# Performance work log

Hardware: AMD Instinct MI355X
Metric: run time of the kernel (lower is better)

Reference implementation:

```python
import jax, jax.numpy as jnp
import numpy as np

H, D_MODEL, D_K, D_V = 16, 1024, 64, 64
IS_DECODE = True


def setup_inputs() -> dict:
    key = jax.random.key(0)
    ks = jax.random.split(key, 6)
    N, L = 4, 2048
    x = jax.random.normal(ks[0], (N, L, D_MODEL), dtype=jnp.float32)
    masked_info = jnp.ones((N, L), dtype=jnp.float32)  # 1 = valid, 0 = pad
    s = 1.0 / np.sqrt(D_MODEL)
    WQ = jax.random.normal(ks[1], (H, D_MODEL, D_K), dtype=jnp.float32) * s
    WK = jax.random.normal(ks[2], (H, D_MODEL, D_K), dtype=jnp.float32) * s
    WV = jax.random.normal(ks[3], (H, D_MODEL, D_V), dtype=jnp.float32) * s
    WO = jax.random.normal(ks[4], (H * D_V, D_MODEL), dtype=jnp.float32) * s
    return {"x": x, "masked_info": masked_info, "WQ": WQ, "WK": WK, "WV": WV, "WO": WO}


def reference(x, masked_info, WQ, WK, WV, WO):
    N, L, _ = x.shape
    scaler = jnp.sqrt(jnp.array(D_K, dtype=x.dtype))
    # per-head projections, batched over heads: [H, N, L, d]
    q = jnp.einsum('nld,hdk->hnlk', x, WQ)
    k = jnp.einsum('nld,hdk->hnlk', x, WK)
    v = jnp.einsum('nld,hdv->hnlv', x, WV)
    scores = jnp.einsum('hnlk,hnmk->hnlm', q, k) / scaler  # [H, N, L, L]
    # outer-product padding mask: True where masked out
    pad_mask = (masked_info[:, :, None] * masked_info[:, None, :]) == 0  # [N, L, L]
    if IS_DECODE:
        causal = jnp.triu(jnp.ones((L, L), dtype=bool), k=1)
        pad_mask = pad_mask | causal[None, :, :]
    scores = jnp.where(pad_mask[None], -jnp.inf, scores)
    attn = jax.nn.softmax(scores, axis=-1)
    attn = jnp.nan_to_num(attn, nan=0.0)  # rows fully masked -> 0
    out_h = jnp.einsum('hnlm,hnmv->hnlv', attn, v)  # [H, N, L, d_v]
    # concat heads along last dim in head order: [N, L, H*d_v]
    concat = jnp.transpose(out_h, (1, 2, 0, 3)).reshape(N, L, H * D_V)
    return concat @ WO
```

## Files before the change

kernel.cpp:

```cpp
#include <hip/hip_runtime.h>
#include <hip/hip_bf16.h>


typedef unsigned short ushort_t;
typedef __bf16 bf16x8 __attribute__((ext_vector_type(8)));
typedef float  f32x4  __attribute__((ext_vector_type(4)));
typedef unsigned short us4 __attribute__((ext_vector_type(4)));
typedef short s16x4 __attribute__((ext_vector_type(4)));

__device__ __forceinline__ ushort_t f2bf(float f) {
    union { float f; unsigned u; } a; a.f = f;
    unsigned r = a.u + 0x7fffu + ((a.u >> 16) & 1u);
    return (ushort_t)(r >> 16);
}

__device__ __forceinline__ void gload16(const ushort_t* g, ushort_t* l) {
    __builtin_amdgcn_global_load_lds(
        (const __attribute__((address_space(1))) void*)g,
        (__attribute__((address_space(3))) void*)l, 16, 0, 0);
}

__global__ __launch_bounds__(256) void cvt_f32_bf16(const float* __restrict__ in,
                                                    ushort_t* __restrict__ out, int n4) {
    int i = blockIdx.x * 256 + threadIdx.x;
    if (i >= n4) return;
    float4 v = reinterpret_cast<const float4*>(in)[i];
    us4 o;
    o[0] = f2bf(v.x); o[1] = f2bf(v.y); o[2] = f2bf(v.z); o[3] = f2bf(v.w);
    reinterpret_cast<us4*>(out)[i] = o;
}

__global__ __launch_bounds__(256) void cvt_transpose(const float* __restrict__ in,
                                                     ushort_t* __restrict__ out,
                                                     int R, int C, int total) {
    int i = blockIdx.x * 256 + threadIdx.x;
    if (i >= total) return;
    int rc = R * C;
    int b = i / rc; int rem = i - b * rc;
    int c = rem / R; int r = rem - c * R;
    out[i] = f2bf(in[(size_t)(b * R + r) * C + c]);
}

template<int MODE>
__global__ __launch_bounds__(256, 2)
void gemm_bt(const ushort_t* __restrict__ Ag, const ushort_t* __restrict__ BT,
             void* __restrict__ Cout, float scale) {
    const int bm = blockIdx.x, by = blockIdx.y;
    const int tid = threadIdx.x;
    const int w = tid >> 6, lane = tid & 63;
    const int g = lane >> 4, c = lane & 15;
    const int m0 = bm * 128;
    const ushort_t* Bbase = BT + (size_t)by * 65536;

    __shared__ __align__(16) ushort_t As[128 * 64];
    __shared__ __align__(16) ushort_t Bs[64 * 64];

    f32x4 acc[2][4];
    #pragma unroll
    for (int i = 0; i < 2; ++i)
        #pragma unroll
        for (int j = 0; j < 4; ++j) acc[i][j] = (f32x4){0.f, 0.f, 0.f, 0.f};

    const int rsub = (w << 3) + (lane >> 3);
    const int s8   = lane & 7;

    for (int t = 0; t < 16; ++t) {
        const int k0 = t * 64;
        #pragma unroll
        for (int is = 0; is < 4; ++is) {
            const int row = is * 32 + rsub;
            gload16(Ag + (size_t)(m0 + row) * 1024 + k0 + ((s8 ^ (row & 7)) << 3),
                    &As[is * 2048 + w * 512]);
        }
        #pragma unroll
        for (int is = 0; is < 2; ++is) {
            const int row = is * 32 + rsub;
            gload16(Bbase + (size_t)row * 1024 + k0 + ((s8 ^ (row & 7)) << 3),
                    &Bs[is * 2048 + w * 512]);
        }
        __syncthreads();
        #pragma unroll
        for (int kk = 0; kk < 2; ++kk) {
            bf16x8 af[2], bfr[4];
            #pragma unroll
            for (int mf = 0; mf < 2; ++mf) {
                const int row = w * 32 + mf * 16 + c;
                const int slot = (kk * 4 + g) ^ (row & 7);
                af[mf] = *reinterpret_cast<const bf16x8*>(&As[row * 64 + slot * 8]);
            }
            #pragma unroll
            for (int nf = 0; nf < 4; ++nf) {
                const int row = nf * 16 + c;
                const int slot = (kk * 4 + g) ^ (row & 7);
                bfr[nf] = *reinterpret_cast<const bf16x8*>(&Bs[row * 64 + slot * 8]);
            }
            __builtin_amdgcn_s_setprio(1);
            #pragma unroll
            for (int mf = 0; mf < 2; ++mf)
                #pragma unroll
                for (int nf = 0; nf < 4; ++nf)
                    acc[mf][nf] = __builtin_amdgcn_mfma_f32_16x16x32_bf16(
                        af[mf], bfr[nf], acc[mf][nf], 0, 0, 0);
            __builtin_amdgcn_s_setprio(0);
        }
        __syncthreads();
    }

    #pragma unroll
    for (int mf = 0; mf < 2; ++mf) {
        const int mbase = m0 + w * 32 + mf * 16 + g * 4;
        #pragma unroll
        for (int nf = 0; nf < 4; ++nf) {
            const int col = nf * 16 + c;
            if (MODE == 3) {
                ushort_t* o = (ushort_t*)Cout + (size_t)by * 524288;
                if (by < 32) {
                    const float scl = (by < 16) ? scale : 1.0f;
                    #pragma unroll
                    for (int r = 0; r < 4; ++r)
                        o[(size_t)(mbase + r) * 64 + col] = f2bf(acc[mf][nf][r] * scl);
                } else {
                    us4 pk;
                    #pragma unroll
                    for (int r = 0; r < 4; ++r) pk[r] = f2bf(acc[mf][nf][r]);
                    const int nIdx = mbase >> 11, l = mbase & 2047;
                    *reinterpret_cast<us4*>(
                        &o[(size_t)nIdx * 131072 + (size_t)col * 2048 + l]) = pk;
                }
            } else {
                float* o = (float*)Cout;
                #pragma unroll
                for (int r = 0; r < 4; ++r)
                    o[(size_t)(mbase + r) * 1024 + by * 64 + col] = acc[mf][nf][r];
            }
        }
    }
}

__global__ __launch_bounds__(256, 4)
void attn_kernel(const ushort_t* __restrict__ qb, const ushort_t* __restrict__ kb,
                 const ushort_t* __restrict__ vtb, const float* __restrict__ mi,
                 ushort_t* __restrict__ cat) {
    const int bx = blockIdx.x;
    const int n = blockIdx.y, h = blockIdx.z;
    const int tid = threadIdx.x;
    const int w = tid >> 6, lane = tid & 63;
    const int g = lane >> 4, c = lane & 15;
    const int qblkA = bx, qblkB = 31 - bx;
    const int q0A = qblkA * 64 + w * 16;
    const int q0B = qblkB * 64 + w * 16;

    const ushort_t* qhn = qb  + (size_t)h * 524288 + (size_t)n * 131072;
    const ushort_t* khn = kb  + (size_t)h * 524288 + (size_t)n * 131072;
    const ushort_t* vhn = vtb + (size_t)h * 524288 + (size_t)n * 131072;
    const float*    mrow = mi + (size_t)n * 2048;

    __shared__ __align__(16) ushort_t Ks[2][64 * 64];
    __shared__ __align__(16) ushort_t Vs[2][64 * 64];

    const int rsub = (w << 3) + (lane >> 3);
    const int s8   = lane & 7;

    auto stage = [&](int jb, int b) {
        const int kbase = jb * 64;
        #pragma unroll
        for (int is = 0; is < 2; ++is) {
            const int row = is * 32 + rsub;
            const int sg  = (s8 ^ (row & 7)) << 3;
            gload16(khn + (size_t)(kbase + row) * 64 + sg, &Ks[b][is * 2048 + w * 512]);
            gload16(vhn + (size_t)row * 2048 + kbase + sg, &Vs[b][is * 2048 + w * 512]);
        }
    };

    bf16x8 qfA[2], qfB[2];
    {
        const ushort_t* qa = qhn + (size_t)(q0A + c) * 64 + g * 8;
        const ushort_t* qb2 = qhn + (size_t)(q0B + c) * 64 + g * 8;
        qfA[0] = *reinterpret_cast<const bf16x8*>(qa);
        qfA[1] = *reinterpret_cast<const bf16x8*>(qa + 32);
        qfB[0] = *reinterpret_cast<const bf16x8*>(qb2);
        qfB[1] = *reinterpret_cast<const bf16x8*>(qb2 + 32);
    }
    const float mqA = mrow[q0A + c];
    const float mqB = mrow[q0B + c];

    float mrunA = -1e30f, lrunA = 0.f, mrunB = -1e30f, lrunB = 0.f;
    f32x4 accA[4], accB[4];
    #pragma unroll
    for (int i = 0; i < 4; ++i) {
        accA[i] = (f32x4){0.f, 0.f, 0.f, 0.f};
        accB[i] = (f32x4){0.f, 0.f, 0.f, 0.f};
    }

    stage(0, 0);
    __syncthreads();
    int buf = 0;

    for (int j = 0; j <= qblkB; ++j) {
        if (j < qblkB) stage(j + 1, buf ^ 1);
        const int kbase = j * 64;
        f32x4 bias[4];
        #pragma unroll
        for (int nf = 0; nf < 4; ++nf) {
            float4 mk = *reinterpret_cast<const float4*>(&mrow[kbase + nf * 16 + g * 4]);
            bias[nf][0] = (mk.x == 0.f) ? -1e30f : 0.f;
            bias[nf][1] = (mk.y == 0.f) ? -1e30f : 0.f;
            bias[nf][2] = (mk.z == 0.f) ? -1e30f : 0.f;
            bias[nf][3] = (mk.w == 0.f) ? -1e30f : 0.f;
        }

        auto do_pass = [&](const bf16x8* qf, f32x4* acc, float& mrun, float& lrun,
                           int q0, bool diag) {
            f32x4 s[4];
            #pragma unroll
            for (int nf = 0; nf < 4; ++nf) s[nf] = (f32x4){0.f, 0.f, 0.f, 0.f};
            __builtin_amdgcn_s_setprio(1);
            #pragma unroll
            for (int kk = 0; kk < 2; ++kk)
                #pragma unroll
                for (int nf = 0; nf < 4; ++nf) {
                    const int row  = nf * 16 + c;
                    const int byte = row * 128 + (((kk * 4 + g) ^ (c & 7)) << 4);
                    bf16x8 kf = *reinterpret_cast<const bf16x8*>(
                        reinterpret_cast<const char*>(&Ks[buf][0]) + byte);
                    s[nf] = __builtin_amdgcn_mfma_f32_16x16x32_bf16(
                        kf, qf[kk], s[nf], 0, 0, 0);
                }
            __builtin_amdgcn_s_setprio(0);
            #pragma unroll
            for (int nf = 0; nf < 4; ++nf) s[nf] += bias[nf];
            if (diag) {
                const int qrow = q0 + c;
                #pragma unroll
                for (int nf = 0; nf < 4; ++nf)
                    #pragma unroll
                    for (int r = 0; r < 4; ++r)
                        if (kbase + nf * 16 + g * 4 + r > qrow) s[nf][r] = -1e30f;
            }
            float m01[4], m23[4];
            #pragma unroll
            for (int r = 0; r < 4; ++r) {
                m01[r] = fmaxf(s[0][r], s[1][r]);
                m23[r] = fmaxf(s[2][r], s[3][r]);
            }
            float mt = fmaxf(fmaxf(fmaxf(m01[0], m01[1]), fmaxf(m01[2], m01[3])),
                             fmaxf(fmaxf(m23[0], m23[1]), fmaxf(m23[2], m23[3])));
            mt = fmaxf(mt, __shfl_xor(mt, 16));
            mt = fmaxf(mt, __shfl_xor(mt, 32));
            if (!__all(mt - mrun <= 8.0f)) {
                const float mnew = fmaxf(mrun, mt);
                const float sc = __builtin_amdgcn_exp2f(mrun - mnew);
                #pragma unroll
                for (int nfd = 0; nfd < 4; ++nfd)
                    #pragma unroll
                    for (int r = 0; r < 4; ++r) acc[nfd][r] *= sc;
                lrun *= sc;
                mrun = mnew;
            }
            float rs = 0.f;
            union { unsigned u[2]; s16x4 v; } pb[4];
            #pragma unroll
            for (int nf = 0; nf < 4; ++nf) {
                const float p0 = __builtin_amdgcn_exp2f(s[nf][0] - mrun);
                const float p1 = __builtin_amdgcn_exp2f(s[nf][1] - mrun);
                const float p2 = __builtin_amdgcn_exp2f(s[nf][2] - mrun);
                const float p3 = __builtin_amdgcn_exp2f(s[nf][3] - mrun);
                rs += (p0 + p1) + (p2 + p3);
                asm("v_cvt_pk_bf16_f32 %0, %1, %2" : "=v"(pb[nf].u[0]) : "v"(p0), "v"(p1));
                asm("v_cvt_pk_bf16_f32 %0, %1, %2" : "=v"(pb[nf].u[1]) : "v"(p2), "v"(p3));
            }
            rs += __shfl_xor(rs, 16);
            rs += __shfl_xor(rs, 32);
            lrun += rs;
            __builtin_amdgcn_s_setprio(1);
            #pragma unroll
            for (int kk = 0; kk < 4; ++kk)
                #pragma unroll
                for (int nfd = 0; nfd < 4; ++nfd) {
                    const int row   = nfd * 16 + c;
                    const int chunk = (kk * 2 + (g >> 1)) ^ (c & 7);
                    const int byte  = row * 128 + (chunk << 4) + (g & 1) * 8;
                    s16x4 vf = *reinterpret_cast<const s16x4*>(
                        reinterpret_cast<const char*>(&Vs[buf][0]) + byte);
                    acc[nfd] = __builtin_amdgcn_mfma_f32_16x16x16bf16_1k(
                        vf, pb[kk].v, acc[nfd], 0, 0, 0);
                }
            __builtin_amdgcn_s_setprio(0);
        };

        if (j <= qblkA) do_pass(qfA, accA, mrunA, lrunA, q0A, j == qblkA);
        do_pass(qfB, accB, mrunB, lrunB, q0B, j == qblkB);

        __syncthreads();
        buf ^= 1;
    }

    auto epi = [&](const f32x4* acc, float mrun, float lrun, float mq, int q0) {
        const float inv = (mq != 0.f && mrun > -1e29f && lrun > 0.f)
                              ? (1.0f / lrun) : 0.f;
        const size_t base = (size_t)(n * 2048 + q0 + c) * 1024 + h * 64;
        #pragma unroll
        for (int nfd = 0; nfd < 4; ++nfd) {
            us4 pk;
            #pragma unroll
            for (int r = 0; r < 4; ++r) pk[r] = f2bf(acc[nfd][r] * inv);
            *reinterpret_cast<us4*>(&cat[base + nfd * 16 + g * 4]) = pk;
        }
    };
    epi(accA, mrunA, lrunA, mqA, q0A);
    epi(accB, mrunB, lrunB, mqB, q0B);
}

extern "C" void kernel_launch(void* const* d_in, const int* in_sizes, int n_in,
                              void* d_out, int out_size, void* d_ws, size_t ws_size,
                              hipStream_t stream) {
    const float* x  = (const float*)d_in[0];
    const float* mi = (const float*)d_in[1];
    const float* WQ = (const float*)d_in[2];
    const float* WK = (const float*)d_in[3];
    const float* WV = (const float*)d_in[4];
    const float* WO = (const float*)d_in[5];
    float* out = (float*)d_out;

    ushort_t* ws  = (ushort_t*)d_ws;
    ushort_t* xb  = ws;
    ushort_t* wqt = xb  + 8388608;
    ushort_t* wkt = wqt + 1048576;
    ushort_t* wvt = wkt + 1048576;
    ushort_t* wot = wvt + 1048576;
    ushort_t* qb  = wot + 1048576;
    ushort_t* kb  = qb  + 8388608;
    ushort_t* vtb = kb  + 8388608;
    ushort_t* cat = xb;

    cvt_f32_bf16<<<8192, 256, 0, stream>>>(x, xb, 2097152);
    cvt_transpose<<<4096, 256, 0, stream>>>(WQ, wqt, 1024, 64, 1048576);
    cvt_transpose<<<4096, 256, 0, stream>>>(WK, wkt, 1024, 64, 1048576);
    cvt_transpose<<<4096, 256, 0, stream>>>(WV, wvt, 1024, 64, 1048576);
    cvt_transpose<<<4096, 256, 0, stream>>>(WO, wot, 1024, 1024, 1048576);

    dim3 g1(64, 48);
    gemm_bt<3><<<g1, 256, 0, stream>>>(xb, wqt, qb, 0.18033688f);

    dim3 g2(16, 4, 16);
    attn_kernel<<<g2, 256, 0, stream>>>(qb, kb, vtb, mi, cat);

    dim3 g3(64, 16);
    gemm_bt<2><<<g3, 256, 0, stream>>>(cat, wot, out, 1.0f);
}
```

Measured before the change: 214.9 us.

## Enlarge GEMM tiles to 128x128 and use tiled shared-memory weight transpose

The GEMM kernel now computes 128x128 output tiles with a 2x2 wave arrangement, each wave holding a 64x64 accumulator block. This halves the grid and doubles operand reuse per loaded tile. The weight convert-transpose kernel is replaced by a 32x32 LDS-tiled version so that global reads and writes are coalesced. The larger accumulator footprint raises register pressure and may lower occupancy.

```diff
diff --git a/kernel.cpp b/kernel.cpp
--- a/kernel.cpp
+++ b/kernel.cpp
@@ -30,15 +30,22 @@
     reinterpret_cast<us4*>(out)[i] = o;
 }
 
-__global__ __launch_bounds__(256) void cvt_transpose(const float* __restrict__ in,
-                                                     ushort_t* __restrict__ out,
-                                                     int R, int C, int total) {
-    int i = blockIdx.x * 256 + threadIdx.x;
-    if (i >= total) return;
-    int rc = R * C;
-    int b = i / rc; int rem = i - b * rc;
-    int c = rem / R; int r = rem - c * R;
-    out[i] = f2bf(in[(size_t)(b * R + r) * C + c]);
+__global__ __launch_bounds__(256) void cvt_transpose32(const float* __restrict__ in,
+                                                       ushort_t* __restrict__ out,
+                                                       int R, int C) {
+    const int b = blockIdx.z;
+    const int c0 = blockIdx.x * 32, r0 = blockIdx.y * 32;
+    const int tx = threadIdx.x & 31, ty = threadIdx.x >> 5;
+    __shared__ ushort_t t[32][33];
+    const float* ip = in + ((size_t)b * R + r0) * C + c0;
+    #pragma unroll
+    for (int i = 0; i < 4; ++i)
+        t[ty + 8 * i][tx] = f2bf(ip[(size_t)(ty + 8 * i) * C + tx]);
+    __syncthreads();
+    ushort_t* op = out + ((size_t)b * C + c0) * R + r0;
+    #pragma unroll
+    for (int i = 0; i < 4; ++i)
+        op[(size_t)(ty + 8 * i) * R + tx] = t[tx][ty + 8 * i];
 }
 
 template<int MODE>
@@ -48,16 +55,17 @@
     const int bm = blockIdx.x, by = blockIdx.y;
     const int tid = threadIdx.x;
     const int w = tid >> 6, lane = tid & 63;
+    const int wr = w >> 1, wc = w & 1;
     const int g = lane >> 4, c = lane & 15;
     const int m0 = bm * 128;
-    const ushort_t* Bbase = BT + (size_t)by * 65536;
+    const ushort_t* Bbase = BT + (size_t)by * 131072;
 
     __shared__ __align__(16) ushort_t As[128 * 64];
-    __shared__ __align__(16) ushort_t Bs[64 * 64];
-
-    f32x4 acc[2][4];
-    #pragma unroll
-    for (int i = 0; i < 2; ++i)
+    __shared__ __align__(16) ushort_t Bs[128 * 64];
+
+    f32x4 acc[4][4];
+    #pragma unroll
+    for (int i = 0; i < 4; ++i)
         #pragma unroll
         for (int j = 0; j < 4; ++j) acc[i][j] = (f32x4){0.f, 0.f, 0.f, 0.f};
 
@@ -69,34 +77,29 @@
         #pragma unroll
         for (int is = 0; is < 4; ++is) {
             const int row = is * 32 + rsub;
-            gload16(Ag + (size_t)(m0 + row) * 1024 + k0 + ((s8 ^ (row & 7)) << 3),
-                    &As[is * 2048 + w * 512]);
-        }
-        #pragma unroll
-        for (int is = 0; is < 2; ++is) {
-            const int row = is * 32 + rsub;
-            gload16(Bbase + (size_t)row * 1024 + k0 + ((s8 ^ (row & 7)) << 3),
-                    &Bs[is * 2048 + w * 512]);
+            const int sg  = (s8 ^ (row & 7)) << 3;
+            gload16(Ag + (size_t)(m0 + row) * 1024 + k0 + sg, &As[is * 2048 + w * 512]);
+            gload16(Bbase + (size_t)row * 1024 + k0 + sg,     &Bs[is * 2048 + w * 512]);
         }
         __syncthreads();
         #pragma unroll
         for (int kk = 0; kk < 2; ++kk) {
-            bf16x8 af[2], bfr[4];
-            #pragma unroll
-            for (int mf = 0; mf < 2; ++mf) {
-                const int row = w * 32 + mf * 16 + c;
+            bf16x8 af[4], bfr[4];
+            #pragma unroll
+            for (int mf = 0; mf < 4; ++mf) {
+                const int row = wr * 64 + mf * 16 + c;
                 const int slot = (kk * 4 + g) ^ (row & 7);
                 af[mf] = *reinterpret_cast<const bf16x8*>(&As[row * 64 + slot * 8]);
             }
             #pragma unroll
             for (int nf = 0; nf < 4; ++nf) {
-                const int row = nf * 16 + c;
+                const int row = wc * 64 + nf * 16 + c;
                 const int slot = (kk * 4 + g) ^ (row & 7);
                 bfr[nf] = *reinterpret_cast<const bf16x8*>(&Bs[row * 64 + slot * 8]);
             }
             __builtin_amdgcn_s_setprio(1);
             #pragma unroll
-            for (int mf = 0; mf < 2; ++mf)
+            for (int mf = 0; mf < 4; ++mf)
                 #pragma unroll
                 for (int nf = 0; nf < 4; ++nf)
                     acc[mf][nf] = __builtin_amdgcn_mfma_f32_16x16x32_bf16(
@@ -107,31 +110,33 @@
     }
 
     #pragma unroll
-    for (int mf = 0; mf < 2; ++mf) {
-        const int mbase = m0 + w * 32 + mf * 16 + g * 4;
+    for (int mf = 0; mf < 4; ++mf) {
+        const int mbase = m0 + wr * 64 + mf * 16 + g * 4;
         #pragma unroll
         for (int nf = 0; nf < 4; ++nf) {
-            const int col = nf * 16 + c;
+            const int colG = wc * 64 + nf * 16 + c;
             if (MODE == 3) {
-                ushort_t* o = (ushort_t*)Cout + (size_t)by * 524288;
-                if (by < 32) {
-                    const float scl = (by < 16) ? scale : 1.0f;
+                const int s  = by * 2 + (colG >> 6);
+                const int c2 = colG & 63;
+                ushort_t* o = (ushort_t*)Cout + (size_t)s * 524288;
+                if (s < 32) {
+                    const float scl = (s < 16) ? scale : 1.0f;
                     #pragma unroll
                     for (int r = 0; r < 4; ++r)
-                        o[(size_t)(mbase + r) * 64 + col] = f2bf(acc[mf][nf][r] * scl);
+                        o[(size_t)(mbase + r) * 64 + c2] = f2bf(acc[mf][nf][r] * scl);
                 } else {
                     us4 pk;
                     #pragma unroll
                     for (int r = 0; r < 4; ++r) pk[r] = f2bf(acc[mf][nf][r]);
                     const int nIdx = mbase >> 11, l = mbase & 2047;
                     *reinterpret_cast<us4*>(
-                        &o[(size_t)nIdx * 131072 + (size_t)col * 2048 + l]) = pk;
+                        &o[(size_t)nIdx * 131072 + (size_t)c2 * 2048 + l]) = pk;
                 }
             } else {
                 float* o = (float*)Cout;
                 #pragma unroll
                 for (int r = 0; r < 4; ++r)
-                    o[(size_t)(mbase + r) * 1024 + by * 64 + col] = acc[mf][nf][r];
+                    o[(size_t)(mbase + r) * 1024 + by * 128 + colG] = acc[mf][nf][r];
             }
         }
     }
@@ -334,17 +339,21 @@
     ushort_t* cat = xb;
 
     cvt_f32_bf16<<<8192, 256, 0, stream>>>(x, xb, 2097152);
-    cvt_transpose<<<4096, 256, 0, stream>>>(WQ, wqt, 1024, 64, 1048576);
-    cvt_transpose<<<4096, 256, 0, stream>>>(WK, wkt, 1024, 64, 1048576);
-    cvt_transpose<<<4096, 256, 0, stream>>>(WV, wvt, 1024, 64, 1048576);
-    cvt_transpose<<<4096, 256, 0, stream>>>(WO, wot, 1024, 1024, 1048576);
-
-    dim3 g1(64, 48);
+    {
+        dim3 gt(2, 32, 16);
+        cvt_transpose32<<<gt, 256, 0, stream>>>(WQ, wqt, 1024, 64);
+        cvt_transpose32<<<gt, 256, 0, stream>>>(WK, wkt, 1024, 64);
+        cvt_transpose32<<<gt, 256, 0, stream>>>(WV, wvt, 1024, 64);
+        dim3 go(32, 32, 1);
+        cvt_transpose32<<<go, 256, 0, stream>>>(WO, wot, 1024, 1024);
+    }
+
+    dim3 g1(64, 24);
     gemm_bt<3><<<g1, 256, 0, stream>>>(xb, wqt, qb, 0.18033688f);
 
     dim3 g2(16, 4, 16);
     attn_kernel<<<g2, 256, 0, stream>>>(qb, kb, vtb, mi, cat);
 
-    dim3 g3(64, 16);
+    dim3 g3(64, 8);
     gemm_bt<2><<<g3, 256, 0, stream>>>(cat, wot, out, 1.0f);
 }
```

Result: faster. 193.1 us (-10.1%).
